# Performance work log

Hardware: AMD Instinct MI355X
Metric: run time of the kernel (lower is better)

The kernel has to match this reference:

```python
import jax, jax.numpy as jnp
import numpy as np

DIM = 256
NUM_HEADS = 8


def setup_inputs() -> dict:
    key = jax.random.key(0)
    ks = jax.random.split(key, 5)
    B, V, C, H, W = 4, 6, DIM, 64, 64
    x = jax.random.normal(ks[0], (B, V, C, H, W), dtype=jnp.float32)
    # 1x1 conv weights (out_channels, in_channels), bias=False
    s = 1.0 / np.sqrt(C)
    Wq = jax.random.normal(ks[1], (C, C), dtype=jnp.float32) * s
    Wk = jax.random.normal(ks[2], (C, C), dtype=jnp.float32) * s
    Wv = jax.random.normal(ks[3], (C, C), dtype=jnp.float32) * s
    Wo = jax.random.normal(ks[4], (C, C), dtype=jnp.float32) * s
    return {"x": x, "Wq": Wq, "Wk": Wk, "Wv": Wv, "Wo": Wo}


def reference(x, Wq, Wk, Wv, Wo):
    B, V, C, H, W = x.shape
    h = NUM_HEADS
    dh = C // h
    scale = dh ** (-0.5)

    def proj(Wm):
        # 1x1 conv == per-pixel channel matmul; -> [B, h, V, HW, dh]
        t = jnp.einsum('bvchw,oc->bvohw', x, Wm)
        t = t.reshape(B, V, h, dh, H * W)
        return t.transpose(0, 2, 1, 4, 3)  # b h v w d (w = flattened HW)

    Q = proj(Wq)
    K = proj(Wk)
    Vv = proj(Wv)

    Qloc = Q.mean(axis=2)  # average query over views: [B, h, HW, dh]
    scores = jnp.einsum('bhwd,bhvwd->bhwv', Qloc, K) * scale  # [B, h, HW, V]
    attn = jax.nn.softmax(scores, axis=-1)
    out = jnp.einsum('bhwv,bhvwd->bhwd', attn, Vv)  # [B, h, HW, dh]
    out = out.transpose(0, 1, 3, 2).reshape(B, C, H, W)
    return jnp.einsum('bchw,oc->bohw', out, Wo)  # out_proj 1x1 conv
```

## Files before the change

kernel.cpp:

```cpp
#include <hip/hip_runtime.h>
#include <hip/hip_bf16.h>


typedef __bf16 bf16x8 __attribute__((ext_vector_type(8)));
typedef float f32x4 __attribute__((ext_vector_type(4)));

#define HW 4096
#define C_DIM 256
#define NV 6
#define NB 4

__global__ __launch_bounds__(256) void convert_weights_kernel(
    const float* __restrict__ Wq, const float* __restrict__ Wk,
    const float* __restrict__ Wv, const float* __restrict__ Wo,
    __hip_bfloat16* __restrict__ out)
{
    const float* srcs[4] = {Wq, Wk, Wv, Wo};
    const int m = blockIdx.y;
    const int i = blockIdx.x * 256 + threadIdx.x;
    out[m * 65536 + i] = __float2bfloat16(srcs[m][i]);
}

__global__ __launch_bounds__(256) void transpose_mean_kernel(
    const float* __restrict__ x,
    __hip_bfloat16* __restrict__ xt,
    __hip_bfloat16* __restrict__ xbar)
{
    __shared__ float tile[64][65];
    const int w0 = blockIdx.x * 64;
    const int c0 = blockIdx.y * 64;
    const int b  = blockIdx.z;
    const int t  = threadIdx.x;
    const int li = t & 63;
    const int qi = t >> 6;
    float acc[16];
#pragma unroll
    for (int i = 0; i < 16; ++i) acc[i] = 0.f;

    for (int v = 0; v < NV; ++v) {
        const float* src = x + (((size_t)b * NV + v) * C_DIM + c0) * HW + w0;
#pragma unroll
        for (int i = 0; i < 16; ++i) {
            const int c = qi + 4 * i;
            tile[li][c] = src[(size_t)c * HW + li];
        }
        __syncthreads();
        __hip_bfloat16* dst = xt + (((size_t)b * NV + v) * HW + w0) * C_DIM + c0;
#pragma unroll
        for (int i = 0; i < 16; ++i) {
            const int w = qi + 4 * i;
            const float val = tile[w][li];
            acc[i] += val;
            dst[(size_t)w * C_DIM + li] = __float2bfloat16(val);
        }
        __syncthreads();
    }
    __hip_bfloat16* dbar = xbar + ((size_t)b * HW + w0) * C_DIM + c0;
#pragma unroll
    for (int i = 0; i < 16; ++i) {
        const int w = qi + 4 * i;
        dbar[(size_t)w * C_DIM + li] = __float2bfloat16(acc[i] * (1.f / 6.f));
    }
}

__global__ __launch_bounds__(512, 2) void mega_kernel(
    const __hip_bfloat16* __restrict__ xt,
    const __hip_bfloat16* __restrict__ xbar,
    const __hip_bfloat16* __restrict__ Wq,
    const __hip_bfloat16* __restrict__ Wk,
    const __hip_bfloat16* __restrict__ Wv,
    const __hip_bfloat16* __restrict__ Wo,
    float* __restrict__ out)
{
    __shared__ __align__(16) __hip_bfloat16 Abuf[2][16384];
    __shared__ float T[64][257];
    const size_t SL = (size_t)HW * C_DIM;
    const int w0 = blockIdx.x * 64;
    const int b  = blockIdx.y;
    const int t  = threadIdx.x, wv = t >> 6, l = t & 63;
    const int kb_l = l >> 4, rl = l & 15;
    const int px = l, h = wv;

    f32x4 acc[4][2];

    auto zacc = [&]() {
#pragma unroll
        for (int i = 0; i < 4; ++i)
#pragma unroll
            for (int j = 0; j < 2; ++j) {
                acc[i][j][0] = 0.f; acc[i][j][1] = 0.f;
                acc[i][j][2] = 0.f; acc[i][j][3] = 0.f;
            }
    };

    auto stageA = [&](int buf, const __hip_bfloat16* src) {
#pragma unroll
        for (int c2 = 0; c2 < 4; ++c2) {
            const int ch = wv * 4 + c2;
            const __hip_bfloat16* g = src + (size_t)(w0 + l) * 256 + ch * 8;
            __builtin_amdgcn_global_load_lds(
                (const __attribute__((address_space(1))) void*)g,
                (__attribute__((address_space(3))) void*)(&Abuf[buf][ch * 512]),
                16, 0, 0);
        }
    };

    auto ldA = [&](int buf, int kt, bf16x8 af[4]) {
#pragma unroll
        for (int i = 0; i < 4; ++i)
            af[i] = *(const bf16x8*)&Abuf[buf][(kt * 4 + kb_l) * 512 + (i * 16 + rl) * 8];
    };

    auto gemmStream = [&](int buf, const __hip_bfloat16* W) {
        const __hip_bfloat16* wb = W + (size_t)(wv * 32 + rl) * 256 + kb_l * 8;
        bf16x8 bcur[2], bnxt[2];
#pragma unroll
        for (int j = 0; j < 2; ++j) bcur[j] = *(const bf16x8*)(wb + j * 16 * 256);
#pragma unroll
        for (int kt = 0; kt < 8; ++kt) {
            if (kt < 7) {
#pragma unroll
                for (int j = 0; j < 2; ++j)
                    bnxt[j] = *(const bf16x8*)(wb + (kt + 1) * 32 + j * 16 * 256);
            }
            bf16x8 af[4]; ldA(buf, kt, af);
#pragma unroll
            for (int i = 0; i < 4; ++i)
#pragma unroll
                for (int j = 0; j < 2; ++j)
                    acc[i][j] = __builtin_amdgcn_mfma_f32_16x16x32_bf16(af[i], bcur[j], acc[i][j], 0, 0, 0);
            bcur[0] = bnxt[0]; bcur[1] = bnxt[1];
        }
    };

    auto writeT = [&]() {
#pragma unroll
        for (int i = 0; i < 4; ++i)
#pragma unroll
            for (int j = 0; j < 2; ++j)
#pragma unroll
                for (int r = 0; r < 4; ++r)
                    T[i * 16 + (l >> 4) * 4 + r][wv * 32 + j * 16 + rl] = acc[i][j][r];
    };

    bf16x8 bkreg[8][2];
#pragma unroll
    for (int kt = 0; kt < 8; ++kt)
#pragma unroll
        for (int j = 0; j < 2; ++j)
            bkreg[kt][j] = *(const bf16x8*)(Wk + (size_t)(wv * 32 + j * 16 + rl) * 256 + kt * 32 + kb_l * 8);

    auto gemmK = [&](int buf) {
#pragma unroll
        for (int kt = 0; kt < 8; ++kt) {
            bf16x8 af[4]; ldA(buf, kt, af);
#pragma unroll
            for (int i = 0; i < 4; ++i)
#pragma unroll
                for (int j = 0; j < 2; ++j)
                    acc[i][j] = __builtin_amdgcn_mfma_f32_16x16x32_bf16(af[i], bkreg[kt][j], acc[i][j], 0, 0, 0);
        }
    };

    stageA(0, xbar + (size_t)b * SL);
    __syncthreads();
    zacc();
    gemmStream(0, Wq);
    stageA(1, xt + (size_t)(b * NV) * SL);
    writeT();
    __syncthreads();

    const float scale = 0.17677669529663687f;
    float q[32];
#pragma unroll
    for (int cc = 0; cc < 32; ++cc) q[cc] = T[px][h * 32 + cc] * scale;

    float m = -1e30f, den = 0.f;
    float o[32];
#pragma unroll
    for (int cc = 0; cc < 32; ++cc) o[cc] = 0.f;

    for (int v = 0; v < NV; ++v) {
        const int buf = (v + 1) & 1;
        __syncthreads();
        zacc();
        gemmK(buf);
        if (v < NV - 1) stageA(buf ^ 1, xt + (size_t)(b * NV + v + 1) * SL);
        writeT();
        __syncthreads();

        float s = 0.f;
#pragma unroll
        for (int cc = 0; cc < 32; ++cc) s += q[cc] * T[px][h * 32 + cc];
        const float mn = fmaxf(m, s);
        const float f  = __expf(m - mn);
        const float e  = __expf(s - mn);
        den = den * f + e;
        m = mn;
#pragma unroll
        for (int cc = 0; cc < 32; ++cc) o[cc] *= f;
        __syncthreads();

        zacc();
        gemmStream(buf, Wv);
        writeT();
        __syncthreads();
#pragma unroll
        for (int cc = 0; cc < 32; ++cc) o[cc] += e * T[px][h * 32 + cc];
    }

    const float inv = 1.f / den;
#pragma unroll
    for (int c2 = 0; c2 < 4; ++c2) {
        bf16x8 ov;
#pragma unroll
        for (int k = 0; k < 8; ++k) ov[k] = (__bf16)(o[c2 * 8 + k] * inv);
        *(bf16x8*)&Abuf[0][(h * 4 + c2) * 512 + px * 8] = ov;
    }
    __syncthreads();
    zacc();
    gemmStream(0, Wo);

    float* op = out + (size_t)b * C_DIM * HW;
#pragma unroll
    for (int i = 0; i < 4; ++i)
#pragma unroll
        for (int j = 0; j < 2; ++j) {
            const int col = wv * 32 + j * 16 + rl;
            *(f32x4*)(op + (size_t)col * HW + w0 + i * 16 + (l >> 4) * 4) = acc[i][j];
        }
}

extern "C" void kernel_launch(void* const* d_in, const int* in_sizes, int n_in,
                              void* d_out, int out_size, void* d_ws, size_t ws_size,
                              hipStream_t stream)
{
    const float* x  = (const float*)d_in[0];
    const float* Wq = (const float*)d_in[1];
    const float* Wk = (const float*)d_in[2];
    const float* Wv = (const float*)d_in[3];
    const float* Wo = (const float*)d_in[4];
    (void)in_sizes; (void)n_in; (void)out_size; (void)ws_size;

    char* ws = (char*)d_ws;
    const size_t MB = 1024ull * 1024ull;
    const size_t SL = (size_t)HW * C_DIM;

    __hip_bfloat16* Wbf  = (__hip_bfloat16*)(ws);
    __hip_bfloat16* xt   = (__hip_bfloat16*)(ws + 1 * MB);
    __hip_bfloat16* xbar = (__hip_bfloat16*)(ws + 49 * MB);

    const __hip_bfloat16* WqB = Wbf;
    const __hip_bfloat16* WkB = Wbf + 65536;
    const __hip_bfloat16* WvB = Wbf + 131072;
    const __hip_bfloat16* WoB = Wbf + 196608;

    convert_weights_kernel<<<dim3(256, 4), 256, 0, stream>>>(Wq, Wk, Wv, Wo, Wbf);
    transpose_mean_kernel<<<dim3(HW / 64, C_DIM / 64, NB), 256, 0, stream>>>(x, xt, xbar);
    mega_kernel<<<dim3(HW / 64, NB), 512, 0, stream>>>(xt, xbar, WqB, WkB, WvB, WoB, (float*)d_out);
}
```

Measured before the change: 98.11 us.

## Keep all weight fragments in registers, transpose T buffer, drop to one block per CU

The fused attention kernel now keeps the Wq, Wk, Wv and Wo MFMA B-fragments in registers instead of streaming Wq, Wv and Wo from global memory in every GEMM. Launch bounds drop to one block per CU so the larger register budget fits. The score/value staging buffer is transposed so each lane writes its accumulator as a vector store, and the scaled query is held in bf16 registers. The next view's async LDS prefetch is issued before the K GEMM instead of after it. The cost is lower occupancy, less latency hiding, and reduced precision in the query dot product.

```diff
diff --git a/kernel.cpp b/kernel.cpp
--- a/kernel.cpp
+++ b/kernel.cpp
@@ -63,7 +63,7 @@
     }
 }
 
-__global__ __launch_bounds__(512, 2) void mega_kernel(
+__global__ __launch_bounds__(512, 1) void mega_kernel(
     const __hip_bfloat16* __restrict__ xt,
     const __hip_bfloat16* __restrict__ xbar,
     const __hip_bfloat16* __restrict__ Wq,
@@ -73,16 +73,15 @@
     float* __restrict__ out)
 {
     __shared__ __align__(16) __hip_bfloat16 Abuf[2][16384];
-    __shared__ float T[64][257];
+    __shared__ __align__(16) float T2[256][68];
     const size_t SL = (size_t)HW * C_DIM;
     const int w0 = blockIdx.x * 64;
     const int b  = blockIdx.y;
     const int t  = threadIdx.x, wv = t >> 6, l = t & 63;
-    const int kb_l = l >> 4, rl = l & 15;
+    const int kb_l = l >> 4, rl = l & 15, lq = l >> 4;
     const int px = l, h = wv;
 
     f32x4 acc[4][2];
-
     auto zacc = [&]() {
 #pragma unroll
         for (int i = 0; i < 4; ++i)
@@ -105,93 +104,81 @@
         }
     };
 
-    auto ldA = [&](int buf, int kt, bf16x8 af[4]) {
+    auto preloadW = [&](const __hip_bfloat16* W, bf16x8 (&fr)[8][2]) {
+#pragma unroll
+        for (int kt = 0; kt < 8; ++kt)
+#pragma unroll
+            for (int j = 0; j < 2; ++j)
+                fr[kt][j] = *(const bf16x8*)(W + (size_t)(wv * 32 + j * 16 + rl) * 256 + kt * 32 + kb_l * 8);
+    };
+
+    auto gemmFrags = [&](int buf, const bf16x8 (&fr)[8][2]) {
+#pragma unroll
+        for (int kt = 0; kt < 8; ++kt) {
+            bf16x8 af[4];
+#pragma unroll
+            for (int i = 0; i < 4; ++i)
+                af[i] = *(const bf16x8*)&Abuf[buf][(kt * 4 + kb_l) * 512 + (i * 16 + rl) * 8];
+#pragma unroll
+            for (int i = 0; i < 4; ++i)
+#pragma unroll
+                for (int j = 0; j < 2; ++j)
+                    acc[i][j] = __builtin_amdgcn_mfma_f32_16x16x32_bf16(af[i], fr[kt][j], acc[i][j], 0, 0, 0);
+        }
+    };
+
+    auto writeT2 = [&]() {
 #pragma unroll
         for (int i = 0; i < 4; ++i)
-            af[i] = *(const bf16x8*)&Abuf[buf][(kt * 4 + kb_l) * 512 + (i * 16 + rl) * 8];
-    };
-
-    auto gemmStream = [&](int buf, const __hip_bfloat16* W) {
-        const __hip_bfloat16* wb = W + (size_t)(wv * 32 + rl) * 256 + kb_l * 8;
-        bf16x8 bcur[2], bnxt[2];
-#pragma unroll
-        for (int j = 0; j < 2; ++j) bcur[j] = *(const bf16x8*)(wb + j * 16 * 256);
-#pragma unroll
-        for (int kt = 0; kt < 8; ++kt) {
-            if (kt < 7) {
-#pragma unroll
-                for (int j = 0; j < 2; ++j)
-                    bnxt[j] = *(const bf16x8*)(wb + (kt + 1) * 32 + j * 16 * 256);
-            }
-            bf16x8 af[4]; ldA(buf, kt, af);
-#pragma unroll
-            for (int i = 0; i < 4; ++i)
-#pragma unroll
-                for (int j = 0; j < 2; ++j)
-                    acc[i][j] = __builtin_amdgcn_mfma_f32_16x16x32_bf16(af[i], bcur[j], acc[i][j], 0, 0, 0);
-            bcur[0] = bnxt[0]; bcur[1] = bnxt[1];
-        }
-    };
-
-    auto writeT = [&]() {
-#pragma unroll
-        for (int i = 0; i < 4; ++i)
 #pragma unroll
             for (int j = 0; j < 2; ++j)
-#pragma unroll
-                for (int r = 0; r < 4; ++r)
-                    T[i * 16 + (l >> 4) * 4 + r][wv * 32 + j * 16 + rl] = acc[i][j][r];
-    };
-
-    bf16x8 bkreg[8][2];
-#pragma unroll
-    for (int kt = 0; kt < 8; ++kt)
-#pragma unroll
-        for (int j = 0; j < 2; ++j)
-            bkreg[kt][j] = *(const bf16x8*)(Wk + (size_t)(wv * 32 + j * 16 + rl) * 256 + kt * 32 + kb_l * 8);
-
-    auto gemmK = [&](int buf) {
-#pragma unroll
-        for (int kt = 0; kt < 8; ++kt) {
-            bf16x8 af[4]; ldA(buf, kt, af);
-#pragma unroll
-            for (int i = 0; i < 4; ++i)
-#pragma unroll
-                for (int j = 0; j < 2; ++j)
-                    acc[i][j] = __builtin_amdgcn_mfma_f32_16x16x32_bf16(af[i], bkreg[kt][j], acc[i][j], 0, 0, 0);
-        }
-    };
+                *(f32x4*)&T2[wv * 32 + j * 16 + rl][i * 16 + lq * 4] = acc[i][j];
+    };
+
+    bf16x8 bkreg[8][2], bvreg[8][2];
 
     stageA(0, xbar + (size_t)b * SL);
+    bf16x8 wqf[8][2];
+    preloadW(Wq, wqf);
+    preloadW(Wk, bkreg);
     __syncthreads();
     zacc();
-    gemmStream(0, Wq);
+    gemmFrags(0, wqf);
     stageA(1, xt + (size_t)(b * NV) * SL);
-    writeT();
+    preloadW(Wv, bvreg);
+    writeT2();
     __syncthreads();
 
     const float scale = 0.17677669529663687f;
-    float q[32];
-#pragma unroll
-    for (int cc = 0; cc < 32; ++cc) q[cc] = T[px][h * 32 + cc] * scale;
+    bf16x8 qbf[4];
+#pragma unroll
+    for (int i = 0; i < 4; ++i)
+#pragma unroll
+        for (int j = 0; j < 8; ++j)
+            qbf[i][j] = (__bf16)(T2[h * 32 + i * 8 + j][px] * scale);
 
     float m = -1e30f, den = 0.f;
     float o[32];
 #pragma unroll
     for (int cc = 0; cc < 32; ++cc) o[cc] = 0.f;
 
+    bf16x8 wof[8][2];
+
     for (int v = 0; v < NV; ++v) {
         const int buf = (v + 1) & 1;
         __syncthreads();
+        if (v < NV - 1) stageA(buf ^ 1, xt + (size_t)(b * NV + v + 1) * SL);
         zacc();
-        gemmK(buf);
-        if (v < NV - 1) stageA(buf ^ 1, xt + (size_t)(b * NV + v + 1) * SL);
-        writeT();
+        gemmFrags(buf, bkreg);
+        writeT2();
         __syncthreads();
 
         float s = 0.f;
 #pragma unroll
-        for (int cc = 0; cc < 32; ++cc) s += q[cc] * T[px][h * 32 + cc];
+        for (int i = 0; i < 4; ++i)
+#pragma unroll
+            for (int j = 0; j < 8; ++j)
+                s += (float)qbf[i][j] * T2[h * 32 + i * 8 + j][px];
         const float mn = fmaxf(m, s);
         const float f  = __expf(m - mn);
         const float e  = __expf(s - mn);
@@ -202,11 +189,12 @@
         __syncthreads();
 
         zacc();
-        gemmStream(buf, Wv);
-        writeT();
-        __syncthreads();
-#pragma unroll
-        for (int cc = 0; cc < 32; ++cc) o[cc] += e * T[px][h * 32 + cc];
+        gemmFrags(buf, bvreg);
+        if (v == NV - 1) preloadW(Wo, wof);
+        writeT2();
+        __syncthreads();
+#pragma unroll
+        for (int cc = 0; cc < 32; ++cc) o[cc] += e * T2[h * 32 + cc][px];
     }
 
     const float inv = 1.f / den;
@@ -219,7 +207,7 @@
     }
     __syncthreads();
     zacc();
-    gemmStream(0, Wo);
+    gemmFrags(0, wof);
 
     float* op = out + (size_t)b * C_DIM * HW;
 #pragma unroll
@@ -227,7 +215,7 @@
 #pragma unroll
         for (int j = 0; j < 2; ++j) {
             const int col = wv * 32 + j * 16 + rl;
-            *(f32x4*)(op + (size_t)col * HW + w0 + i * 16 + (l >> 4) * 4) = acc[i][j];
+            *(f32x4*)(op + (size_t)col * HW + w0 + i * 16 + lq * 4) = acc[i][j];
         }
 }
 
```

Result: no change. 96.61 us (-1.5%).
